# Optimization experiments

Measured on AMD Instinct MI355X. Metric: run time of the kernel, lower is better.

## Reference

```python
import jax, jax.numpy as jnp
import numpy as np

B, T = 4096, 2048

def setup_inputs() -> dict:
    key = jax.random.key(0)
    k1, k2, k3 = jax.random.split(key, 3)
    pred = jax.random.normal(k1, (B, T), dtype=jnp.float32)  # predicted log-durations
    # alignment = ground-truth durations (strictly positive, log is taken)
    alignment = jax.random.uniform(k2, (B, T), dtype=jnp.float32, minval=1.0, maxval=20.0)
    token_lengths = jax.random.randint(k3, (B,), 1, T + 1)  # valid lengths in [1, T]
    return {"pred": pred, "alignment": alignment, "token_lengths": token_lengths}

def reference(pred, alignment, token_lengths):
    # Masked per-sample MSE over the first token_lengths[i] positions,
    # then mean over the batch (matches the python loop exactly).
    Tdim = pred.shape[1]
    mask = jnp.arange(Tdim)[None, :] < token_lengths[:, None]          # [B, T] bool
    diff = jnp.where(mask, pred - jnp.log(alignment), 0.0)             # padded alignment > 0, log is safe
    per_sample_mse = jnp.sum(diff * diff, axis=1) / token_lengths.astype(pred.dtype)  # [B]
    return jnp.mean(per_sample_mse)
```

## Files before the change

### kernel.cpp

```cpp
#include <hip/hip_runtime.h>


__global__ __launch_bounds__(256) void dploss_row_kernel(
    const float* __restrict__ pred,
    const float* __restrict__ align,
    const int* __restrict__ lens,
    float* __restrict__ row_out,
    int T)
{
    const int row = blockIdx.x;
    const int L = lens[row];
    const float4* __restrict__ p4 = (const float4*)(pred + (size_t)row * T);
    const float4* __restrict__ a4 = (const float4*)(align + (size_t)row * T);
    const int ngroups = (L + 3) >> 2;

    float acc = 0.0f;
    for (int g = threadIdx.x; g < ngroups; g += 256) {
        float4 p = p4[g];
        float4 a = a4[g];
        const int base = g << 2;
        if (base + 4 <= L) {
            float d0 = p.x - __logf(a.x);
            float d1 = p.y - __logf(a.y);
            float d2 = p.z - __logf(a.z);
            float d3 = p.w - __logf(a.w);
            acc += d0 * d0 + d1 * d1 + d2 * d2 + d3 * d3;
        } else {
            if (base + 0 < L) { float d = p.x - __logf(a.x); acc += d * d; }
            if (base + 1 < L) { float d = p.y - __logf(a.y); acc += d * d; }
            if (base + 2 < L) { float d = p.z - __logf(a.z); acc += d * d; }
        }
    }

    #pragma unroll
    for (int off = 32; off > 0; off >>= 1)
        acc += __shfl_down(acc, off, 64);

    __shared__ float wsum[4];
    const int lane = threadIdx.x & 63;
    const int wave = threadIdx.x >> 6;
    if (lane == 0) wsum[wave] = acc;
    __syncthreads();
    if (threadIdx.x == 0) {
        float total = wsum[0] + wsum[1] + wsum[2] + wsum[3];
        row_out[row] = total / (float)L;
    }
}

__global__ __launch_bounds__(256) void dploss_mean_kernel(
    const float* __restrict__ row_out,
    float* __restrict__ out,
    int B)
{
    float acc = 0.0f;
    for (int i = threadIdx.x; i < B; i += 256)
        acc += row_out[i];

    #pragma unroll
    for (int off = 32; off > 0; off >>= 1)
        acc += __shfl_down(acc, off, 64);

    __shared__ float wsum[4];
    const int lane = threadIdx.x & 63;
    const int wave = threadIdx.x >> 6;
    if (lane == 0) wsum[wave] = acc;
    __syncthreads();
    if (threadIdx.x == 0)
        out[0] = (wsum[0] + wsum[1] + wsum[2] + wsum[3]) / (float)B;
}

extern "C" void kernel_launch(void* const* d_in, const int* in_sizes, int n_in,
                              void* d_out, int out_size, void* d_ws, size_t ws_size,
                              hipStream_t stream)
{
    const float* pred  = (const float*)d_in[0];
    const float* align = (const float*)d_in[1];
    const int*   lens  = (const int*)d_in[2];

    const int B = in_sizes[2];
    const int T = in_sizes[0] / B;

    float* row_out = (float*)d_ws;
    float* out     = (float*)d_out;

    dploss_row_kernel<<<B, 256, 0, stream>>>(pred, align, lens, row_out, T);
    dploss_mean_kernel<<<1, 256, 0, stream>>>(row_out, out, B);
}
```

Baseline: 98.42 us.

## Fuse row and mean reductions into one wave-per-row kernel with atomic accumulation

Each 64-lane wave now handles one row instead of a 256-thread block per row, with eight rows packed per 512-thread block. Each block sums its rows' MSEs and adds them to the output with an atomicAdd, which replaces the second single-block mean kernel; a memset zeroes the output first. This removes the launch and serialized tail of the mean kernel and the per-row block synchronization. In exchange each row is streamed by only 64 lanes, so rows of varying length load-balance differently, and the float atomics make the summation order nondeterministic.

```diff
diff --git a/kernel.cpp b/kernel.cpp
--- a/kernel.cpp
+++ b/kernel.cpp
@@ -1,72 +1,62 @@
 #include <hip/hip_runtime.h>
 
 
-__global__ __launch_bounds__(256) void dploss_row_kernel(
+__global__ __launch_bounds__(512) void dploss_fused_kernel(
     const float* __restrict__ pred,
     const float* __restrict__ align,
     const int* __restrict__ lens,
-    float* __restrict__ row_out,
-    int T)
+    float* __restrict__ out,
+    int B, int T)
 {
-    const int row = blockIdx.x;
-    const int L = lens[row];
-    const float4* __restrict__ p4 = (const float4*)(pred + (size_t)row * T);
-    const float4* __restrict__ a4 = (const float4*)(align + (size_t)row * T);
-    const int ngroups = (L + 3) >> 2;
+    const int gtid = blockIdx.x * blockDim.x + threadIdx.x;
+    const int wave = gtid >> 6;
+    const int lane = threadIdx.x & 63;
+    const int wave_in_block = threadIdx.x >> 6;
 
-    float acc = 0.0f;
-    for (int g = threadIdx.x; g < ngroups; g += 256) {
-        float4 p = p4[g];
-        float4 a = a4[g];
-        const int base = g << 2;
-        if (base + 4 <= L) {
-            float d0 = p.x - __logf(a.x);
-            float d1 = p.y - __logf(a.y);
-            float d2 = p.z - __logf(a.z);
-            float d3 = p.w - __logf(a.w);
-            acc += d0 * d0 + d1 * d1 + d2 * d2 + d3 * d3;
-        } else {
-            if (base + 0 < L) { float d = p.x - __logf(a.x); acc += d * d; }
-            if (base + 1 < L) { float d = p.y - __logf(a.y); acc += d * d; }
-            if (base + 2 < L) { float d = p.z - __logf(a.z); acc += d * d; }
+    float row_mse = 0.0f;
+
+    if (wave < B) {
+        const int row = wave;
+        const int L = lens[row];
+        const float4* __restrict__ p4 = (const float4*)(pred + (size_t)row * T);
+        const float4* __restrict__ a4 = (const float4*)(align + (size_t)row * T);
+        const int ngroups = (L + 3) >> 2;
+
+        float acc = 0.0f;
+        for (int g = lane; g < ngroups; g += 64) {
+            float4 p = p4[g];
+            float4 a = a4[g];
+            const int base = g << 2;
+            if (base + 4 <= L) {
+                float d0 = p.x - __logf(a.x);
+                float d1 = p.y - __logf(a.y);
+                float d2 = p.z - __logf(a.z);
+                float d3 = p.w - __logf(a.w);
+                acc += d0 * d0 + d1 * d1 + d2 * d2 + d3 * d3;
+            } else {
+                if (base + 0 < L) { float d = p.x - __logf(a.x); acc += d * d; }
+                if (base + 1 < L) { float d = p.y - __logf(a.y); acc += d * d; }
+                if (base + 2 < L) { float d = p.z - __logf(a.z); acc += d * d; }
+            }
         }
+
+        #pragma unroll
+        for (int off = 32; off > 0; off >>= 1)
+            acc += __shfl_down(acc, off, 64);
+
+        row_mse = acc / (float)L;
     }
 
-    #pragma unroll
-    for (int off = 32; off > 0; off >>= 1)
-        acc += __shfl_down(acc, off, 64);
+    __shared__ float wsum[8];
+    if (lane == 0) wsum[wave_in_block] = row_mse;
+    __syncthreads();
 
-    __shared__ float wsum[4];
-    const int lane = threadIdx.x & 63;
-    const int wave = threadIdx.x >> 6;
-    if (lane == 0) wsum[wave] = acc;
-    __syncthreads();
     if (threadIdx.x == 0) {
-        float total = wsum[0] + wsum[1] + wsum[2] + wsum[3];
-        row_out[row] = total / (float)L;
+        float total = 0.0f;
+        #pragma unroll
+        for (int w = 0; w < 8; ++w) total += wsum[w];
+        atomicAdd(out, total / (float)B);
     }
-}
-
-__global__ __launch_bounds__(256) void dploss_mean_kernel(
-    const float* __restrict__ row_out,
-    float* __restrict__ out,
-    int B)
-{
-    float acc = 0.0f;
-    for (int i = threadIdx.x; i < B; i += 256)
-        acc += row_out[i];
-
-    #pragma unroll
-    for (int off = 32; off > 0; off >>= 1)
-        acc += __shfl_down(acc, off, 64);
-
-    __shared__ float wsum[4];
-    const int lane = threadIdx.x & 63;
-    const int wave = threadIdx.x >> 6;
-    if (lane == 0) wsum[wave] = acc;
-    __syncthreads();
-    if (threadIdx.x == 0)
-        out[0] = (wsum[0] + wsum[1] + wsum[2] + wsum[3]) / (float)B;
 }
 
 extern "C" void kernel_launch(void* const* d_in, const int* in_sizes, int n_in,
@@ -80,9 +70,13 @@
     const int B = in_sizes[2];
     const int T = in_sizes[0] / B;
 
-    float* row_out = (float*)d_ws;
-    float* out     = (float*)d_out;
+    float* out = (float*)d_out;
 
-    dploss_row_kernel<<<B, 256, 0, stream>>>(pred, align, lens, row_out, T);
-    dploss_mean_kernel<<<1, 256, 0, stream>>>(row_out, out, B);
+    hipMemsetAsync(out, 0, sizeof(float), stream);
+
+    const int threads = 512;
+    const int waves_per_block = threads / 64;
+    const int grid = (B + waves_per_block - 1) / waves_per_block;
+
+    dploss_fused_kernel<<<grid, threads, 0, stream>>>(pred, align, lens, out, B, T);
 }
```

Result: no change. 96.64 us (-1.8%).
